# Kernel optimization log

Hardware: AMD Instinct MI355X
Metric: run time of the kernel (lower is better)

## Reference

```python
import jax, jax.numpy as jnp
import numpy as np

IN_DIM = 2048
OUT_DIM = 1536
N_PARAM = max(IN_DIM, OUT_DIM)  # 2048


def setup_inputs() -> dict:
    key = jax.random.key(0)
    k1, k2, k3 = jax.random.split(key, 3)
    x = jax.random.normal(k1, (8, 64, 64, IN_DIM), dtype=jnp.float32)
    # NOTE: original init is zeros for W_first_col (output would be all-zero);
    # we use randn so the reference computes something non-trivial.
    W_first_col = jax.random.normal(k2, (N_PARAM,), dtype=jnp.float32)
    W_second_col = jax.random.normal(k3, (N_PARAM,), dtype=jnp.float32)
    return {"x": x, "W_first_col": W_first_col, "W_second_col": W_second_col}


def reference(x, W_first_col, W_second_col):
    # Effective first column of the circulant matrix, truncated to in_dim
    W = (W_first_col * W_second_col)[:IN_DIM]            # [C]
    W_fft = jnp.fft.fft(W)                               # [C] complex64
    x_fft = jnp.fft.fft(x, axis=-1)                      # [B,H,W,C] complex64
    result = jnp.fft.ifft(W_fft * x_fft, axis=-1).real   # circular conv along channels
    return result[..., :OUT_DIM]                         # [B,H,W,out_dim]
```

## Files before the change

kernel.cpp:

```cpp
#include <hip/hip_runtime.h>
#include <math.h>

#define C_LEN 2048
#define HALF  1024
#define OUTD  1536
#define NPIX  32768
#define LDSW  1088

#define FENCE() __builtin_amdgcn_sched_barrier(0)

__device__ __forceinline__ int SWZ(int idx) { return idx ^ ((idx >> 5) & 31); }

template<int DIR>
__device__ void fft2048(float* r0, float* i0, float* r1, float* i1, int t) {
    float *sr = r0, *si = i0, *dr = r1, *di = i1;
    const float TW = (float)DIR * 6.283185307179586f / 2048.0f;
    const float FD = (float)DIR;
    __syncthreads();
    #pragma unroll
    for (int b = 0; b < 4; ++b) {
        int t2 = t + b * 256;
        float ar = sr[SWZ(t2)],        ai = si[SWZ(t2)];
        float br = sr[SWZ(t2 + 1024)], bi = si[SWZ(t2 + 1024)];
        float sn, cs;
        sincosf(TW * (float)t2, &sn, &cs);
        float vr = ar - br, vi = ai - bi;
        int w0 = 2 * t2;
        dr[SWZ(w0)]     = ar + br;
        di[SWZ(w0)]     = ai + bi;
        dr[SWZ(w0 + 1)] = cs * vr - sn * vi;
        di[SWZ(w0 + 1)] = cs * vi + sn * vr;
    }
    { float* tp; tp = sr; sr = dr; dr = tp; tp = si; si = di; di = tp; }
    #pragma unroll
    for (int m = 2; m <= 512; m *= 4) {
        __syncthreads();
        #pragma unroll
        for (int b = 0; b < 2; ++b) {
            int t2 = t + b * 256;
            int jm = t2 & ~(m - 1);
            float a0r = sr[SWZ(t2)],        a0i = si[SWZ(t2)];
            float a1r = sr[SWZ(t2 + 512)],  a1i = si[SWZ(t2 + 512)];
            float a2r = sr[SWZ(t2 + 1024)], a2i = si[SWZ(t2 + 1024)];
            float a3r = sr[SWZ(t2 + 1536)], a3i = si[SWZ(t2 + 1536)];
            float s0r = a0r + a2r, s0i = a0i + a2i;
            float d0r = a0r - a2r, d0i = a0i - a2i;
            float s1r = a1r + a3r, s1i = a1i + a3i;
            float d1r = a1r - a3r, d1i = a1i - a3i;
            float A0r = s0r + s1r, A0i = s0i + s1i;
            float A2r = s0r - s1r, A2i = s0i - s1i;
            float A1r = d0r - FD * d1i, A1i = d0i + FD * d1r;
            float A3r = d0r + FD * d1i, A3i = d0i - FD * d1r;
            float s1w, c1w;
            sincosf(TW * (float)jm, &s1w, &c1w);
            float c2w = c1w * c1w - s1w * s1w, s2w = 2.0f * c1w * s1w;
            float c3w = c1w * c2w - s1w * s2w, s3w = c1w * s2w + s1w * c2w;
            int wb = t2 + 3 * jm;
            dr[SWZ(wb)]         = A0r;
            di[SWZ(wb)]         = A0i;
            dr[SWZ(wb + m)]     = c1w * A1r - s1w * A1i;
            di[SWZ(wb + m)]     = c1w * A1i + s1w * A1r;
            dr[SWZ(wb + 2 * m)] = c2w * A2r - s2w * A2i;
            di[SWZ(wb + 2 * m)] = c2w * A2i + s2w * A2r;
            dr[SWZ(wb + 3 * m)] = c3w * A3r - s3w * A3i;
            di[SWZ(wb + 3 * m)] = c3w * A3i + s3w * A3r;
        }
        { float* tp; tp = sr; sr = dr; dr = tp; tp = si; si = di; di = tp; }
    }
    __syncthreads();
}

__global__ __launch_bounds__(256)
void uv_kernel(const float* __restrict__ w1, const float* __restrict__ w2,
               float4* __restrict__ uv) {
    __shared__ float r0[C_LEN], i0[C_LEN], r1[C_LEN], i1[C_LEN];
    int t = threadIdx.x;
    #pragma unroll
    for (int k = 0; k < 8; ++k) {
        int e = t + k * 256;
        r0[SWZ(e)] = w1[e] * w2[e];
        i0[SWZ(e)] = 0.0f;
    }
    fft2048<-1>(r0, i0, r1, i1, t);
    #pragma unroll
    for (int b = 0; b < 4; ++b) {
        int k = t + b * 256;
        float w1r = r0[SWZ(k)],        w1i = i0[SWZ(k)];
        float w2r = r0[SWZ(k + 1024)], w2i = i0[SWZ(k + 1024)];
        float Sr = (w1r + w2r) * (1.0f / 4096.0f);
        float Si = (w1i + w2i) * (1.0f / 4096.0f);
        float Dr = (w1r - w2r) * (1.0f / 4096.0f);
        float Di = (w1i - w2i) * (1.0f / 4096.0f);
        float sn, cs;
        sincosf((6.283185307179586f / 2048.0f) * (float)k, &sn, &cs);
        float Er = cs * Dr - sn * Di, Ei = cs * Di + sn * Dr;
        float Fr = cs * Dr + sn * Di, Fi = cs * Di - sn * Dr;
        uv[k] = make_float4(Sr - Ei, Si + Er, Sr + Fi, Si - Fr);
    }
}

__device__ __forceinline__ void cm(float& or_, float& oi_, float ar, float ai,
                                   float br, float bi) {
    or_ = ar * br - ai * bi;
    oi_ = ar * bi + ai * br;
}

template<int S>
__device__ __forceinline__ void fft16_ip(float* xr, float* xi) {
    const float FS = (float)S;
    const float C1 = 0.9238795325112867f;
    const float S1 = 0.3826834323650898f;
    const float R2 = 0.7071067811865476f;
    #pragma unroll
    for (int n0 = 0; n0 < 4; ++n0) {
        float a0r = xr[n0],      a0i = xi[n0];
        float a1r = xr[n0 + 4],  a1i = xi[n0 + 4];
        float a2r = xr[n0 + 8],  a2i = xi[n0 + 8];
        float a3r = xr[n0 + 12], a3i = xi[n0 + 12];
        float t0r = a0r + a2r, t0i = a0i + a2i;
        float t1r = a0r - a2r, t1i = a0i - a2i;
        float t2r = a1r + a3r, t2i = a1i + a3i;
        float t3r = a1r - a3r, t3i = a1i - a3i;
        float y1r = t1r - FS * t3i, y1i = t1i + FS * t3r;
        float y2r = t0r - t2r,      y2i = t0i - t2i;
        float y3r = t1r + FS * t3i, y3i = t1i - FS * t3r;
        xr[n0] = t0r + t2r;  xi[n0] = t0i + t2i;
        if (n0 == 0) {
            xr[4]  = y1r; xi[4]  = y1i;
            xr[8]  = y2r; xi[8]  = y2i;
            xr[12] = y3r; xi[12] = y3i;
        } else if (n0 == 1) {
            cm(xr[5],  xi[5],  y1r, y1i, C1,  FS * S1);
            cm(xr[9],  xi[9],  y2r, y2i, R2,  FS * R2);
            cm(xr[13], xi[13], y3r, y3i, S1,  FS * C1);
        } else if (n0 == 2) {
            cm(xr[6],  xi[6],  y1r, y1i, R2,  FS * R2);
            xr[10] = -FS * y2i;  xi[10] = FS * y2r;
            cm(xr[14], xi[14], y3r, y3i, -R2, FS * R2);
        } else {
            cm(xr[7],  xi[7],  y1r, y1i, S1,  FS * C1);
            cm(xr[11], xi[11], y2r, y2i, -R2, FS * R2);
            cm(xr[15], xi[15], y3r, y3i, -C1, -FS * S1);
        }
    }
    #pragma unroll
    for (int k0 = 0; k0 < 4; ++k0) {
        float b0r = xr[4 * k0],     b0i = xi[4 * k0];
        float b1r = xr[4 * k0 + 1], b1i = xi[4 * k0 + 1];
        float b2r = xr[4 * k0 + 2], b2i = xi[4 * k0 + 2];
        float b3r = xr[4 * k0 + 3], b3i = xi[4 * k0 + 3];
        float t0r = b0r + b2r, t0i = b0i + b2i;
        float t1r = b0r - b2r, t1i = b0i - b2i;
        float t2r = b1r + b3r, t2i = b1i + b3i;
        float t3r = b1r - b3r, t3i = b1i - b3i;
        xr[4 * k0]     = t0r + t2r;      xi[4 * k0]     = t0i + t2i;
        xr[4 * k0 + 1] = t1r - FS * t3i; xi[4 * k0 + 1] = t1i + FS * t3r;
        xr[4 * k0 + 2] = t0r - t2r;      xi[4 * k0 + 2] = t0i - t2i;
        xr[4 * k0 + 3] = t1r + FS * t3i; xi[4 * k0 + 3] = t1i - FS * t3r;
    }
}

__device__ __forceinline__ void tw_store(const float* vr, const float* vi,
                                         float2* row, int xorv, float th) {
    float bs, bc;
    __sincosf(th, &bs, &bc);
    float aR[4], aI[4], bR[4], bI[4];
    aR[0] = 1.f; aI[0] = 0.f;
    aR[1] = bc;  aI[1] = bs;
    aR[2] = bc * bc - bs * bs;          aI[2] = 2.f * bc * bs;
    aR[3] = aR[2] * bc - aI[2] * bs;    aI[3] = aR[2] * bs + aI[2] * bc;
    bR[0] = 1.f; bI[0] = 0.f;
    bR[1] = aR[2] * aR[2] - aI[2] * aI[2];  bI[1] = 2.f * aR[2] * aI[2];
    bR[2] = bR[1] * bR[1] - bI[1] * bI[1];  bI[2] = 2.f * bR[1] * bI[1];
    bR[3] = bR[2] * bR[1] - bI[2] * bI[1];  bI[3] = bR[2] * bI[1] + bI[2] * bR[1];
    #pragma unroll
    for (int c = 0; c < 16; ++c) {
        int p = ((c & 3) << 2) | (c >> 2);
        float x0 = vr[p], y0 = vi[p];
        float x1 = x0 * aR[c & 3] - y0 * aI[c & 3];
        float y1 = x0 * aI[c & 3] + y0 * aR[c & 3];
        float x2 = x1 * bR[c >> 2] - y1 * bI[c >> 2];
        float y2 = x1 * bI[c >> 2] + y1 * bR[c >> 2];
        row[c ^ xorv] = make_float2(x2, y2);
    }
}

__global__ __launch_bounds__(128, 4)
void conv128(const float* __restrict__ x, const float4* __restrict__ uv,
             float2* __restrict__ out) {
    __shared__ float2 ldsAll[2 * LDSW];
    const int tid = threadIdx.x;
    const int t   = tid & 63;
    const int wid = tid >> 6;
    float2* lds = ldsAll + wid * LDSW;
    const size_t pix = ((size_t)blockIdx.x << 1) + wid;
    const float2* xp = reinterpret_cast<const float2*>(x) + pix * (size_t)HALF;

    float vr[16], vi[16];
    #pragma unroll
    for (int a = 0; a < 16; ++a) {
        float2 z = xp[(a << 6) + t];
        vr[a] = z.x; vi[a] = z.y;
    }

    fft16_ip<-1>(vr, vi);
    tw_store(vr, vi, lds + t * 17, 0,
             (-6.283185307179586f / 1024.0f) * (float)t);
    FENCE();
    {
        const int f = t & 3, c = t >> 2;
        const float2* rp = lds + f * 17 + c;
        #pragma unroll
        for (int e = 0; e < 16; ++e) {
            float2 z = rp[e * 68];
            vr[e] = z.x; vi[e] = z.y;
        }
        FENCE();
        fft16_ip<-1>(vr, vi);
        tw_store(vr, vi, lds + (t << 4), c,
                 (-6.283185307179586f / 64.0f) * (float)f);
    }
    FENCE();
    {
        const int q = t & 3, c = t >> 2;
        float dr[16], di[16];
        #pragma unroll
        for (int f = 0; f < 4; ++f) {
            #pragma unroll
            for (int s = 0; s < 4; ++s) {
                int wrow = (c << 2) + f;
                float2 z = lds[(wrow << 4) + (((q << 2) + s) ^ c)];
                dr[f * 4 + s] = z.x; di[f * 4 + s] = z.y;
            }
        }
        FENCE();
        #pragma unroll
        for (int s = 0; s < 4; ++s) {
            float ar = dr[0 + s],  ai = di[0 + s];
            float br = dr[4 + s],  bi = di[4 + s];
            float cr = dr[8 + s],  ci = di[8 + s];
            float er = dr[12 + s], ei = di[12 + s];
            float t0r = ar + cr, t0i = ai + ci;
            float t1r = ar - cr, t1i = ai - ci;
            float t2r = br + er, t2i = bi + ei;
            float t3r = br - er, t3i = bi - ei;
            int kb = c + (q << 6) + (s << 4);
            lds[kb]       = make_float2(t0r + t2r, t0i + t2i);
            lds[kb + 256] = make_float2(t1r + t3i, t1i - t3r);
            lds[kb + 512] = make_float2(t0r - t2r, t0i - t2i);
            lds[kb + 768] = make_float2(t1r - t3i, t1i + t3r);
        }
    }
    FENCE();

    #pragma unroll
    for (int a = 0; a < 16; ++a) {
        int k = (a << 6) + t;
        float2 Za = lds[k];
        float2 Zm = lds[(HALF - k) & (HALF - 1)];
        float4 u  = uv[k];
        float Ar = Za.x + Zm.x, Ai = Za.y - Zm.y;
        float Br = Za.x - Zm.x, Bi = Za.y + Zm.y;
        vr[a] = Ar * u.x - Ai * u.y + Br * u.z - Bi * u.w;
        vi[a] = Ar * u.y + Ai * u.x + Br * u.w + Bi * u.z;
    }
    FENCE();

    fft16_ip<1>(vr, vi);
    tw_store(vr, vi, lds + t * 17, 0,
             (6.283185307179586f / 1024.0f) * (float)t);
    FENCE();
    {
        const int f = t & 3, c = t >> 2;
        const float2* rp = lds + f * 17 + c;
        #pragma unroll
        for (int e = 0; e < 16; ++e) {
            float2 z = rp[e * 68];
            vr[e] = z.x; vi[e] = z.y;
        }
        FENCE();
        fft16_ip<1>(vr, vi);
        tw_store(vr, vi, lds + (t << 4), c,
                 (6.283185307179586f / 64.0f) * (float)f);
    }
    FENCE();
    {
        const int q = t & 3, c = t >> 2;
        float dr[16], di[16];
        #pragma unroll
        for (int f = 0; f < 4; ++f) {
            #pragma unroll
            for (int s = 0; s < 4; ++s) {
                int wrow = (c << 2) + f;
                float2 z = lds[(wrow << 4) + (((q << 2) + s) ^ c)];
                dr[f * 4 + s] = z.x; di[f * 4 + s] = z.y;
            }
        }
        float2* op = out + pix * (size_t)(OUTD / 2);
        #pragma unroll
        for (int s = 0; s < 4; ++s) {
            float ar = dr[0 + s],  ai = di[0 + s];
            float br = dr[4 + s],  bi = di[4 + s];
            float cr = dr[8 + s],  ci = di[8 + s];
            float er = dr[12 + s], ei = di[12 + s];
            float t0r = ar + cr, t0i = ai + ci;
            float t1r = ar - cr, t1i = ai - ci;
            float t2r = br + er, t2i = bi + ei;
            float t3r = br - er, t3i = bi - ei;
            int nb = c + (q << 6) + (s << 4);
            op[nb]       = make_float2(t0r + t2r, t0i + t2i);
            op[nb + 256] = make_float2(t1r - t3i, t1i + t3r);
            op[nb + 512] = make_float2(t0r - t2r, t0i - t2i);
        }
    }
}

extern "C" void kernel_launch(void* const* d_in, const int* in_sizes, int n_in,
                              void* d_out, int out_size, void* d_ws, size_t ws_size,
                              hipStream_t stream) {
    const float* x  = (const float*)d_in[0];
    const float* w1 = (const float*)d_in[1];
    const float* w2 = (const float*)d_in[2];
    float2* out = (float2*)d_out;
    float4* uv  = (float4*)d_ws;

    hipLaunchKernelGGL(uv_kernel, dim3(1), dim3(256), 0, stream, w1, w2, uv);
    hipLaunchKernelGGL(conv128, dim3(NPIX / 2), dim3(128), 0, stream, x, uv, out);
}
```

Before: 130.1 us.

## Process two pixels per wavefront with float4 LDS interleaving and shared twiddles

Each 64-thread block now handles two pixels in one wavefront instead of two wavefronts each handling one pixel. The two pixels' complex values are interleaved as float4 in LDS, so every LDS access moves twice the data, and twiddle factors plus the uv spectrum loads are computed once and shared by both pixels. The twiddle application is also restructured to precompute a combined twiddle. This doubles register pressure per thread (four 16-element arrays), which may lower occupancy or cause spills, and the launch bounds change to 64 threads with 2 blocks per unit.

```diff
diff --git a/kernel.cpp b/kernel.cpp
--- a/kernel.cpp
+++ b/kernel.cpp
@@ -160,8 +160,9 @@
     }
 }
 
-__device__ __forceinline__ void tw_store(const float* vr, const float* vi,
-                                         float2* row, int xorv, float th) {
+__device__ __forceinline__ void tw_store2(const float* vrA, const float* viA,
+                                          const float* vrB, const float* viB,
+                                          float4* row, int xorv, float th) {
     float bs, bc;
     __sincosf(th, &bs, &bc);
     float aR[4], aI[4], bR[4], bI[4];
@@ -176,79 +177,97 @@
     #pragma unroll
     for (int c = 0; c < 16; ++c) {
         int p = ((c & 3) << 2) | (c >> 2);
-        float x0 = vr[p], y0 = vi[p];
-        float x1 = x0 * aR[c & 3] - y0 * aI[c & 3];
-        float y1 = x0 * aI[c & 3] + y0 * aR[c & 3];
-        float x2 = x1 * bR[c >> 2] - y1 * bI[c >> 2];
-        float y2 = x1 * bI[c >> 2] + y1 * bR[c >> 2];
-        row[c ^ xorv] = make_float2(x2, y2);
-    }
-}
-
-__global__ __launch_bounds__(128, 4)
-void conv128(const float* __restrict__ x, const float4* __restrict__ uv,
-             float2* __restrict__ out) {
-    __shared__ float2 ldsAll[2 * LDSW];
-    const int tid = threadIdx.x;
-    const int t   = tid & 63;
-    const int wid = tid >> 6;
-    float2* lds = ldsAll + wid * LDSW;
-    const size_t pix = ((size_t)blockIdx.x << 1) + wid;
-    const float2* xp = reinterpret_cast<const float2*>(x) + pix * (size_t)HALF;
-
-    float vr[16], vi[16];
+        float wr = aR[c & 3] * bR[c >> 2] - aI[c & 3] * bI[c >> 2];
+        float wi = aR[c & 3] * bI[c >> 2] + aI[c & 3] * bR[c >> 2];
+        float xA = vrA[p] * wr - viA[p] * wi;
+        float yA = vrA[p] * wi + viA[p] * wr;
+        float xB = vrB[p] * wr - viB[p] * wi;
+        float yB = vrB[p] * wi + viB[p] * wr;
+        row[c ^ xorv] = make_float4(xA, yA, xB, yB);
+    }
+}
+
+__global__ __launch_bounds__(64, 2)
+void conv64x2(const float* __restrict__ x, const float4* __restrict__ uv,
+              float2* __restrict__ out) {
+    __shared__ float4 lds[LDSW];
+    const int t = threadIdx.x;
+    const size_t pixA = (size_t)blockIdx.x << 1;
+    const float2* xpA = reinterpret_cast<const float2*>(x) + pixA * (size_t)HALF;
+    const float2* xpB = xpA + HALF;
+
+    float vrA[16], viA[16], vrB[16], viB[16];
     #pragma unroll
     for (int a = 0; a < 16; ++a) {
-        float2 z = xp[(a << 6) + t];
-        vr[a] = z.x; vi[a] = z.y;
-    }
-
-    fft16_ip<-1>(vr, vi);
-    tw_store(vr, vi, lds + t * 17, 0,
-             (-6.283185307179586f / 1024.0f) * (float)t);
+        float2 zA = xpA[(a << 6) + t];
+        float2 zB = xpB[(a << 6) + t];
+        vrA[a] = zA.x; viA[a] = zA.y;
+        vrB[a] = zB.x; viB[a] = zB.y;
+    }
+
+    fft16_ip<-1>(vrA, viA);
+    fft16_ip<-1>(vrB, viB);
+    tw_store2(vrA, viA, vrB, viB, lds + t * 17, 0,
+              (-6.283185307179586f / 1024.0f) * (float)t);
     FENCE();
     {
         const int f = t & 3, c = t >> 2;
-        const float2* rp = lds + f * 17 + c;
+        const float4* rp = lds + f * 17 + c;
         #pragma unroll
         for (int e = 0; e < 16; ++e) {
-            float2 z = rp[e * 68];
-            vr[e] = z.x; vi[e] = z.y;
+            float4 z = rp[e * 68];
+            vrA[e] = z.x; viA[e] = z.y; vrB[e] = z.z; viB[e] = z.w;
         }
         FENCE();
-        fft16_ip<-1>(vr, vi);
-        tw_store(vr, vi, lds + (t << 4), c,
-                 (-6.283185307179586f / 64.0f) * (float)f);
+        fft16_ip<-1>(vrA, viA);
+        fft16_ip<-1>(vrB, viB);
+        tw_store2(vrA, viA, vrB, viB, lds + (t << 4), c,
+                  (-6.283185307179586f / 64.0f) * (float)f);
     }
     FENCE();
     {
         const int q = t & 3, c = t >> 2;
-        float dr[16], di[16];
-        #pragma unroll
-        for (int f = 0; f < 4; ++f) {
+        float drA[16], diA[16], drB[16], diB[16];
+        #pragma unroll
+        for (int f2 = 0; f2 < 4; ++f2) {
             #pragma unroll
             for (int s = 0; s < 4; ++s) {
-                int wrow = (c << 2) + f;
-                float2 z = lds[(wrow << 4) + (((q << 2) + s) ^ c)];
-                dr[f * 4 + s] = z.x; di[f * 4 + s] = z.y;
+                int wrow = (c << 2) + f2;
+                float4 z = lds[(wrow << 4) + (((q << 2) + s) ^ c)];
+                drA[f2 * 4 + s] = z.x; diA[f2 * 4 + s] = z.y;
+                drB[f2 * 4 + s] = z.z; diB[f2 * 4 + s] = z.w;
             }
         }
         FENCE();
         #pragma unroll
         for (int s = 0; s < 4; ++s) {
-            float ar = dr[0 + s],  ai = di[0 + s];
-            float br = dr[4 + s],  bi = di[4 + s];
-            float cr = dr[8 + s],  ci = di[8 + s];
-            float er = dr[12 + s], ei = di[12 + s];
-            float t0r = ar + cr, t0i = ai + ci;
-            float t1r = ar - cr, t1i = ai - ci;
-            float t2r = br + er, t2i = bi + ei;
-            float t3r = br - er, t3i = bi - ei;
             int kb = c + (q << 6) + (s << 4);
-            lds[kb]       = make_float2(t0r + t2r, t0i + t2i);
-            lds[kb + 256] = make_float2(t1r + t3i, t1i - t3r);
-            lds[kb + 512] = make_float2(t0r - t2r, t0i - t2i);
-            lds[kb + 768] = make_float2(t1r - t3i, t1i + t3r);
+            {
+                float ar = drA[0 + s],  ai = diA[0 + s];
+                float br = drA[4 + s],  bi = diA[4 + s];
+                float cr = drA[8 + s],  ci = diA[8 + s];
+                float er = drA[12 + s], ei = diA[12 + s];
+                float t0r = ar + cr, t0i = ai + ci;
+                float t1r = ar - cr, t1i = ai - ci;
+                float t2r = br + er, t2i = bi + ei;
+                float t3r = br - er, t3i = bi - ei;
+                float Br = drB[0 + s],  Bi = diB[0 + s];
+                float Cr = drB[4 + s],  Ci = diB[4 + s];
+                float Dr = drB[8 + s],  Di = diB[8 + s];
+                float Er = drB[12 + s], Ei = diB[12 + s];
+                float u0r = Br + Dr, u0i = Bi + Di;
+                float u1r = Br - Dr, u1i = Bi - Di;
+                float u2r = Cr + Er, u2i = Ci + Ei;
+                float u3r = Cr - Er, u3i = Ci - Ei;
+                lds[kb]       = make_float4(t0r + t2r, t0i + t2i,
+                                            u0r + u2r, u0i + u2i);
+                lds[kb + 256] = make_float4(t1r + t3i, t1i - t3r,
+                                            u1r + u3i, u1i - u3r);
+                lds[kb + 512] = make_float4(t0r - t2r, t0i - t2i,
+                                            u0r - u2r, u0i - u2i);
+                lds[kb + 768] = make_float4(t1r - t3i, t1i + t3r,
+                                            u1r - u3i, u1i + u3r);
+            }
         }
     }
     FENCE();
@@ -256,61 +275,88 @@
     #pragma unroll
     for (int a = 0; a < 16; ++a) {
         int k = (a << 6) + t;
-        float2 Za = lds[k];
-        float2 Zm = lds[(HALF - k) & (HALF - 1)];
+        float4 Za = lds[k];
+        float4 Zm = lds[(HALF - k) & (HALF - 1)];
         float4 u  = uv[k];
-        float Ar = Za.x + Zm.x, Ai = Za.y - Zm.y;
-        float Br = Za.x - Zm.x, Bi = Za.y + Zm.y;
-        vr[a] = Ar * u.x - Ai * u.y + Br * u.z - Bi * u.w;
-        vi[a] = Ar * u.y + Ai * u.x + Br * u.w + Bi * u.z;
-    }
-    FENCE();
-
-    fft16_ip<1>(vr, vi);
-    tw_store(vr, vi, lds + t * 17, 0,
-             (6.283185307179586f / 1024.0f) * (float)t);
+        {
+            float Ar = Za.x + Zm.x, Ai = Za.y - Zm.y;
+            float Br = Za.x - Zm.x, Bi = Za.y + Zm.y;
+            vrA[a] = Ar * u.x - Ai * u.y + Br * u.z - Bi * u.w;
+            viA[a] = Ar * u.y + Ai * u.x + Br * u.w + Bi * u.z;
+        }
+        {
+            float Ar = Za.z + Zm.z, Ai = Za.w - Zm.w;
+            float Br = Za.z - Zm.z, Bi = Za.w + Zm.w;
+            vrB[a] = Ar * u.x - Ai * u.y + Br * u.z - Bi * u.w;
+            viB[a] = Ar * u.y + Ai * u.x + Br * u.w + Bi * u.z;
+        }
+    }
+    FENCE();
+
+    fft16_ip<1>(vrA, viA);
+    fft16_ip<1>(vrB, viB);
+    tw_store2(vrA, viA, vrB, viB, lds + t * 17, 0,
+              (6.283185307179586f / 1024.0f) * (float)t);
     FENCE();
     {
         const int f = t & 3, c = t >> 2;
-        const float2* rp = lds + f * 17 + c;
+        const float4* rp = lds + f * 17 + c;
         #pragma unroll
         for (int e = 0; e < 16; ++e) {
-            float2 z = rp[e * 68];
-            vr[e] = z.x; vi[e] = z.y;
+            float4 z = rp[e * 68];
+            vrA[e] = z.x; viA[e] = z.y; vrB[e] = z.z; viB[e] = z.w;
         }
         FENCE();
-        fft16_ip<1>(vr, vi);
-        tw_store(vr, vi, lds + (t << 4), c,
-                 (6.283185307179586f / 64.0f) * (float)f);
+        fft16_ip<1>(vrA, viA);
+        fft16_ip<1>(vrB, viB);
+        tw_store2(vrA, viA, vrB, viB, lds + (t << 4), c,
+                  (6.283185307179586f / 64.0f) * (float)f);
     }
     FENCE();
     {
         const int q = t & 3, c = t >> 2;
-        float dr[16], di[16];
-        #pragma unroll
-        for (int f = 0; f < 4; ++f) {
+        float drA[16], diA[16], drB[16], diB[16];
+        #pragma unroll
+        for (int f2 = 0; f2 < 4; ++f2) {
             #pragma unroll
             for (int s = 0; s < 4; ++s) {
-                int wrow = (c << 2) + f;
-                float2 z = lds[(wrow << 4) + (((q << 2) + s) ^ c)];
-                dr[f * 4 + s] = z.x; di[f * 4 + s] = z.y;
-            }
-        }
-        float2* op = out + pix * (size_t)(OUTD / 2);
+                int wrow = (c << 2) + f2;
+                float4 z = lds[(wrow << 4) + (((q << 2) + s) ^ c)];
+                drA[f2 * 4 + s] = z.x; diA[f2 * 4 + s] = z.y;
+                drB[f2 * 4 + s] = z.z; diB[f2 * 4 + s] = z.w;
+            }
+        }
+        float2* opA = out + pixA * (size_t)(OUTD / 2);
+        float2* opB = opA + (OUTD / 2);
         #pragma unroll
         for (int s = 0; s < 4; ++s) {
-            float ar = dr[0 + s],  ai = di[0 + s];
-            float br = dr[4 + s],  bi = di[4 + s];
-            float cr = dr[8 + s],  ci = di[8 + s];
-            float er = dr[12 + s], ei = di[12 + s];
-            float t0r = ar + cr, t0i = ai + ci;
-            float t1r = ar - cr, t1i = ai - ci;
-            float t2r = br + er, t2i = bi + ei;
-            float t3r = br - er, t3i = bi - ei;
             int nb = c + (q << 6) + (s << 4);
-            op[nb]       = make_float2(t0r + t2r, t0i + t2i);
-            op[nb + 256] = make_float2(t1r - t3i, t1i + t3r);
-            op[nb + 512] = make_float2(t0r - t2r, t0i - t2i);
+            {
+                float ar = drA[0 + s],  ai = diA[0 + s];
+                float br = drA[4 + s],  bi = diA[4 + s];
+                float cr = drA[8 + s],  ci = diA[8 + s];
+                float er = drA[12 + s], ei = diA[12 + s];
+                float t0r = ar + cr, t0i = ai + ci;
+                float t1r = ar - cr, t1i = ai - ci;
+                float t2r = br + er, t2i = bi + ei;
+                float t3r = br - er, t3i = bi - ei;
+                opA[nb]       = make_float2(t0r + t2r, t0i + t2i);
+                opA[nb + 256] = make_float2(t1r - t3i, t1i + t3r);
+                opA[nb + 512] = make_float2(t0r - t2r, t0i - t2i);
+            }
+            {
+                float ar = drB[0 + s],  ai = diB[0 + s];
+                float br = drB[4 + s],  bi = diB[4 + s];
+                float cr = drB[8 + s],  ci = diB[8 + s];
+                float er = drB[12 + s], ei = diB[12 + s];
+                float t0r = ar + cr, t0i = ai + ci;
+                float t1r = ar - cr, t1i = ai - ci;
+                float t2r = br + er, t2i = bi + ei;
+                float t3r = br - er, t3i = bi - ei;
+                opB[nb]       = make_float2(t0r + t2r, t0i + t2i);
+                opB[nb + 256] = make_float2(t1r - t3i, t1i + t3r);
+                opB[nb + 512] = make_float2(t0r - t2r, t0i - t2i);
+            }
         }
     }
 }
@@ -325,5 +371,5 @@
     float4* uv  = (float4*)d_ws;
 
     hipLaunchKernelGGL(uv_kernel, dim3(1), dim3(256), 0, stream, w1, w2, uv);
-    hipLaunchKernelGGL(conv128, dim3(NPIX / 2), dim3(128), 0, stream, x, uv, out);
-}
+    hipLaunchKernelGGL(conv64x2, dim3(NPIX / 2), dim3(64), 0, stream, x, uv, out);
+}
```

Result: no change. 128.6 us (-1.2%).
